# Performance work log

Measured on AMD Instinct MI355X. Metric: run time of the kernel, lower is better.

## Reference

```python
import jax, jax.numpy as jnp
import numpy as np

B, T, D, N = 32, 2048, 1024, 1024  # batch, time, feature dim, n_dense


def setup_inputs() -> dict:
    key = jax.random.key(0)
    ks = jax.random.split(key, 8)
    s = 1.0 / np.sqrt(D)
    return {
        "query": jax.random.normal(ks[0], (B, D), jnp.float32),
        "values": jax.random.normal(ks[1], (B, T, D), jnp.float32),
        "W1": jax.random.uniform(ks[2], (D, N), jnp.float32, -s, s),
        "b1": jnp.zeros((N,), jnp.float32),
        "W2": jax.random.uniform(ks[3], (D, N), jnp.float32, -s, s),
        "b2": jnp.zeros((N,), jnp.float32),
        "V": jax.random.uniform(ks[4], (N, 1), jnp.float32, -1.0 / np.sqrt(N), 1.0 / np.sqrt(N)),
        "bV": jnp.zeros((1,), jnp.float32),
    }


def reference(query, values, W1, b1, W2, b2, V, bV):
    # q_proj: [B, 1, N], v_proj: [B, T, N]
    q_proj = (query @ W1 + b1)[:, None, :]
    v_proj = jnp.einsum("btd,dn->btn", values, W2) + b2
    # score: [B, T, 1]
    score = jnp.tanh(q_proj + v_proj) @ V + bV
    attention_weights = jax.nn.softmax(score, axis=1)  # softmax over time
    # context: [B, D]
    context_vector = jnp.sum(attention_weights * values, axis=1)
    return (context_vector, attention_weights)
```

## Files before the change

### kernel.cpp

```cpp
#include <hip/hip_runtime.h>
#include <hip/hip_bf16.h>

#define B_ 32
#define T_ 2048
#define D_ 1024
#define N_ 1024
#define M_ (B_*T_)

#define BM 64
#define BN 128
#define BK 64
#define NTSPLIT 2
#define NTP (N_ / BN / NTSPLIT)
#define NSTEP (NTP * (D_ / BK))

typedef short bf16x8 __attribute__((ext_vector_type(8)));
typedef float f32x4 __attribute__((ext_vector_type(4)));
typedef unsigned short us4 __attribute__((ext_vector_type(4)));

__device__ __forceinline__ unsigned short bf16_rn(float x) {
    unsigned u = __float_as_uint(x);
    u += 0x7FFFu + ((u >> 16) & 1u);
    return (unsigned short)(u >> 16);
}

__device__ __forceinline__ void gload_lds16(const void* g, void* l) {
    __builtin_amdgcn_global_load_lds(
        (__attribute__((address_space(1))) void*)(g),
        (__attribute__((address_space(3))) void*)(l), 16, 0, 0);
}

__global__ void k0_w2t(const float* __restrict__ W2,
                       unsigned short* __restrict__ Th) {
    __shared__ float tile[32][33];
    int n0 = blockIdx.x * 32, d0 = blockIdx.y * 32;
    int tx = threadIdx.x & 31, ty = threadIdx.x >> 5;
    #pragma unroll
    for (int i = 0; i < 4; i++) {
        int d = d0 + ty + i * 8;
        tile[ty + i * 8][tx] = W2[d * N_ + n0 + tx];
    }
    __syncthreads();
    #pragma unroll
    for (int i = 0; i < 4; i++) {
        int n = n0 + ty + i * 8;
        Th[n * D_ + d0 + tx] = bf16_rn(tile[tx][ty + i * 8]);
    }
}

__global__ void k0_vals(const float* __restrict__ v,
                        unsigned short* __restrict__ o) {
    size_t i = ((size_t)blockIdx.x * 256 + threadIdx.x) * 8;
    const size_t stride = (size_t)gridDim.x * 256 * 8;
    for (; i < (size_t)M_ * D_; i += stride) {
        float4 a = *(const float4*)(v + i);
        float4 b = *(const float4*)(v + i + 4);
        us4 h0, h1;
        h0[0] = bf16_rn(a.x); h0[1] = bf16_rn(a.y);
        h0[2] = bf16_rn(a.z); h0[3] = bf16_rn(a.w);
        h1[0] = bf16_rn(b.x); h1[1] = bf16_rn(b.y);
        h1[2] = bf16_rn(b.z); h1[3] = bf16_rn(b.w);
        *(us4*)(o + i) = h0;
        *(us4*)(o + i + 4) = h1;
    }
}

__global__ void k1_qproj(const float* __restrict__ query,
                         const float* __restrict__ W1,
                         const float* __restrict__ b1,
                         float* __restrict__ qp) {
    int b = blockIdx.x;
    int n = blockIdx.y * 256 + threadIdx.x;
    const float* q = query + b * D_;
    const float* w = W1 + n;
    float s = 0.f;
    #pragma unroll 8
    for (int d = 0; d < D_; d++) s += q[d] * w[d * N_];
    qp[b * N_ + n] = s + b1[n];
}

__device__ __forceinline__ void k2_stage(int u, unsigned short* sa, unsigned short* sb,
                                         int m0, int nt0, int wid, int b_rl, int b_j,
                                         const unsigned short* __restrict__ Av,
                                         const unsigned short* __restrict__ W2Th) {
    const int nt = nt0 + (u >> 4);
    const int k0 = (u & 15) * BK;
    #pragma unroll
    for (int i = 0; i < 4; i++) {
        int r = wid * 32 + i * 8 + b_rl;
        int jj = b_j ^ (r & 7);
        size_t soff = (size_t)(nt * BN + r) * D_ + k0 + jj * 8;
        gload_lds16(W2Th + soff, &sb[(wid * 32 + i * 8) * 64]);
    }
    #pragma unroll
    for (int i = 0; i < 2; i++) {
        int r = wid * 16 + i * 8 + b_rl;
        int jj = b_j ^ (r & 7);
        size_t soff = (size_t)(m0 + r) * D_ + k0 + jj * 8;
        gload_lds16(Av + soff, &sa[(wid * 16 + i * 8) * 64]);
    }
}

__global__ __launch_bounds__(256, 2) void k2_score(
    const unsigned short* __restrict__ Av,
    const unsigned short* __restrict__ W2Th,
    const float* __restrict__ qp,
    const float* __restrict__ b2,
    const float* __restrict__ V,
    float* __restrict__ scorep) {
    __shared__ unsigned short sA[2][BM * BK];
    __shared__ unsigned short sB[2][BN * BK];
    __shared__ float red[2 * BM];

    const int tid = threadIdx.x;
    const int lane = tid & 63;
    const int wid = tid >> 6;
    const int wm = wid >> 1, wn = wid & 1;
    const int g = lane >> 4, c16 = lane & 15;

    const int bid = blockIdx.x;
    const int wgid = ((bid & 7) << 8) | (bid >> 3);
    const int m0 = (wgid >> 1) * BM;
    const int b = m0 >> 11;
    const int half = wgid & 1;
    const int nt0 = half * NTP;

    const int b_rl = lane >> 3;
    const int b_j = lane & 7;

    float rowpart[8];
    #pragma unroll
    for (int i = 0; i < 8; i++) rowpart[i] = 0.f;

    f32x4 acc[2][4];
    #pragma unroll
    for (int mi = 0; mi < 2; mi++)
        #pragma unroll
        for (int ni = 0; ni < 4; ni++) {
            f32x4 z = {0.f, 0.f, 0.f, 0.f};
            acc[mi][ni] = z;
        }

    k2_stage(0, sA[0], sB[0], m0, nt0, wid, b_rl, b_j, Av, W2Th);
    __syncthreads();

    for (int u = 0; u < NSTEP; ++u) {
        const int cur = u & 1;

        if (u + 1 < NSTEP)
            k2_stage(u + 1, sA[cur ^ 1], sB[cur ^ 1], m0, nt0, wid, b_rl, b_j, Av, W2Th);

        #pragma unroll
        for (int s = 0; s < 2; s++) {
            bf16x8 aH[2], bH[4];
            #pragma unroll
            for (int mi = 0; mi < 2; mi++) {
                int r = wm * 32 + mi * 16 + c16;
                int idx = r * 64 + (((s * 4 + g) ^ (r & 7)) << 3);
                aH[mi] = *(const bf16x8*)&sA[cur][idx];
            }
            #pragma unroll
            for (int ni = 0; ni < 4; ni++) {
                int r = wn * 64 + ni * 16 + c16;
                int idx = r * 64 + (((s * 4 + g) ^ (r & 7)) << 3);
                bH[ni] = *(const bf16x8*)&sB[cur][idx];
            }
            #pragma unroll
            for (int mi = 0; mi < 2; mi++)
                #pragma unroll
                for (int ni = 0; ni < 4; ni++)
                    acc[mi][ni] = __builtin_amdgcn_mfma_f32_16x16x32_bf16(aH[mi], bH[ni], acc[mi][ni], 0, 0, 0);
        }

        if ((u & 15) == 15) {
            int nt = nt0 + (u >> 4);
            #pragma unroll
            for (int ni = 0; ni < 4; ni++) {
                int n = nt * BN + wn * 64 + ni * 16 + c16;
                float qv = qp[b * N_ + n] + b2[n];
                float Vv = V[n];
                #pragma unroll
                for (int mi = 0; mi < 2; mi++)
                    #pragma unroll
                    for (int r = 0; r < 4; r++)
                        rowpart[mi * 4 + r] += tanhf(acc[mi][ni][r] + qv) * Vv;
            }
            #pragma unroll
            for (int mi = 0; mi < 2; mi++)
                #pragma unroll
                for (int ni = 0; ni < 4; ni++) {
                    f32x4 z = {0.f, 0.f, 0.f, 0.f};
                    acc[mi][ni] = z;
                }
        }

        __syncthreads();
    }

    #pragma unroll
    for (int i = 0; i < 8; i++) {
        float v = rowpart[i];
        v += __shfl_xor(v, 1);
        v += __shfl_xor(v, 2);
        v += __shfl_xor(v, 4);
        v += __shfl_xor(v, 8);
        rowpart[i] = v;
    }
    if (c16 == 0) {
        #pragma unroll
        for (int mi = 0; mi < 2; mi++)
            #pragma unroll
            for (int r = 0; r < 4; r++)
                red[wn * BM + wm * 32 + mi * 16 + g * 4 + r] = rowpart[mi * 4 + r];
    }
    __syncthreads();
    if (tid < BM) {
        scorep[(size_t)half * M_ + m0 + tid] = red[tid] + red[BM + tid];
    }
}

__global__ void k3_softmax(const float* __restrict__ sp,
                           float* __restrict__ sw) {
    int b = blockIdx.x;
    const float* r0 = sp + b * T_;
    const float* r1 = sp + M_ + b * T_;
    float* row = sw + b * T_;
    int tid = threadIdx.x;
    float v[8];
    float lmax = -1e30f;
    #pragma unroll
    for (int i = 0; i < 8; i++) {
        int idx = tid + i * 256;
        v[i] = r0[idx] + r1[idx];
        lmax = fmaxf(lmax, v[i]);
    }
    #pragma unroll
    for (int d = 1; d < 64; d <<= 1) lmax = fmaxf(lmax, __shfl_xor(lmax, d));
    __shared__ float sm[4], ss[4];
    if ((tid & 63) == 0) sm[tid >> 6] = lmax;
    __syncthreads();
    lmax = fmaxf(fmaxf(sm[0], sm[1]), fmaxf(sm[2], sm[3]));
    float lsum = 0.f;
    #pragma unroll
    for (int i = 0; i < 8; i++) {
        v[i] = expf(v[i] - lmax);
        lsum += v[i];
    }
    #pragma unroll
    for (int d = 1; d < 64; d <<= 1) lsum += __shfl_xor(lsum, d);
    if ((tid & 63) == 0) ss[tid >> 6] = lsum;
    __syncthreads();
    lsum = ss[0] + ss[1] + ss[2] + ss[3];
    float inv = 1.f / lsum;
    #pragma unroll
    for (int i = 0; i < 8; i++) row[tid + i * 256] = v[i] * inv;
}

__global__ void k4_context(const unsigned short* __restrict__ Av,
                           const float* __restrict__ w,
                           float* __restrict__ ctx) {
    int b = blockIdx.x;
    int dc = blockIdx.y;
    int tc = blockIdx.z;
    int d4 = threadIdx.x & 31;
    int th = threadIdx.x >> 5;
    const float* wrow = w + b * T_;
    int d = dc * 128 + d4 * 4;
    const unsigned short* vbase = Av + (size_t)b * T_ * D_ + d;
    float4 acc = {0.f, 0.f, 0.f, 0.f};
    int t0 = tc * 256 + th * 32;
    for (int t = t0; t < t0 + 32; t++) {
        float wt = wrow[t];
        us4 hv = *(const us4*)(vbase + (size_t)t * D_);
        acc.x += wt * __uint_as_float((unsigned)hv[0] << 16);
        acc.y += wt * __uint_as_float((unsigned)hv[1] << 16);
        acc.z += wt * __uint_as_float((unsigned)hv[2] << 16);
        acc.w += wt * __uint_as_float((unsigned)hv[3] << 16);
    }
    __shared__ float4 red4[256];
    red4[threadIdx.x] = acc;
    __syncthreads();
    if (th == 0) {
        float4 s = red4[d4];
        #pragma unroll
        for (int i = 1; i < 8; i++) {
            float4 o = red4[i * 32 + d4];
            s.x += o.x; s.y += o.y; s.z += o.z; s.w += o.w;
        }
        atomicAdd(&ctx[b * D_ + d + 0], s.x);
        atomicAdd(&ctx[b * D_ + d + 1], s.y);
        atomicAdd(&ctx[b * D_ + d + 2], s.z);
        atomicAdd(&ctx[b * D_ + d + 3], s.w);
    }
}

extern "C" void kernel_launch(void* const* d_in, const int* in_sizes, int n_in,
                              void* d_out, int out_size, void* d_ws, size_t ws_size,
                              hipStream_t stream) {
    const float* query  = (const float*)d_in[0];
    const float* values = (const float*)d_in[1];
    const float* W1     = (const float*)d_in[2];
    const float* b1     = (const float*)d_in[3];
    const float* W2     = (const float*)d_in[4];
    const float* b2     = (const float*)d_in[5];
    const float* V      = (const float*)d_in[6];

    float* ctx = (float*)d_out;
    float* weights = (float*)d_out + B_ * D_;

    size_t need = (size_t)N_ * D_ * sizeof(unsigned short)
                + (size_t)B_ * N_ * sizeof(float)
                + (size_t)NTSPLIT * M_ * sizeof(float)
                + (size_t)M_ * D_ * sizeof(unsigned short);
    if (ws_size < need) return;
    unsigned short* Th = (unsigned short*)d_ws;
    float* qp = (float*)(Th + (size_t)N_ * D_);
    float* scorep = qp + (size_t)B_ * N_;
    unsigned short* Av = (unsigned short*)(scorep + (size_t)NTSPLIT * M_);

    k0_w2t<<<dim3(N_ / 32, D_ / 32), 256, 0, stream>>>(W2, Th);
    k0_vals<<<2048, 256, 0, stream>>>(values, Av);
    k1_qproj<<<dim3(B_, N_ / 256), 256, 0, stream>>>(query, W1, b1, qp);
    k2_score<<<(M_ / BM) * NTSPLIT, 256, 0, stream>>>(Av, Th, qp, b2, V, scorep);
    k3_softmax<<<B_, 256, 0, stream>>>(scorep, weights);
    hipMemsetAsync(ctx, 0, (size_t)B_ * D_ * sizeof(float), stream);
    k4_context<<<dim3(B_, 8, 8), 256, 0, stream>>>(Av, weights, ctx);
}
```

Baseline: 395.7 us.

## Triple-buffer score GEMM with BK=32 and merge prep kernels and memset

The score GEMM moves from a double-buffered BK=64 loop with a full __syncthreads to a triple-buffered BK=32 pipeline. It uses explicit vmcnt waits and raw barriers so two global-to-LDS loads stay in flight while MFMAs run, and the LDS swizzle changes to suit 32-wide rows. The W2 transpose and q-projection are fused into one prep kernel, and the context memset moves into the softmax kernel, which removes launches. The smaller K step doubles the number of barriers and loop iterations, and there is a redundant dead LDS read left in the B-fragment load.

Result: no change. 399.4 us (+0.9%).

```diff
diff --git a/kernel.cpp b/kernel.cpp
--- a/kernel.cpp
+++ b/kernel.cpp
@@ -9,7 +9,7 @@
 
 #define BM 64
 #define BN 128
-#define BK 64
+#define BK 32
 #define NTSPLIT 2
 #define NTP (N_ / BN / NTSPLIT)
 #define NSTEP (NTP * (D_ / BK))
@@ -30,21 +30,40 @@
         (__attribute__((address_space(3))) void*)(l), 16, 0, 0);
 }
 
-__global__ void k0_w2t(const float* __restrict__ W2,
-                       unsigned short* __restrict__ Th) {
+#define FENCE() asm volatile("" ::: "memory")
+#define RAW_BARRIER() do { FENCE(); __builtin_amdgcn_s_barrier(); FENCE(); } while (0)
+
+__global__ void k_prep(const float* __restrict__ W2, unsigned short* __restrict__ Th,
+                       const float* __restrict__ query, const float* __restrict__ W1,
+                       const float* __restrict__ b1, float* __restrict__ qp) {
     __shared__ float tile[32][33];
-    int n0 = blockIdx.x * 32, d0 = blockIdx.y * 32;
-    int tx = threadIdx.x & 31, ty = threadIdx.x >> 5;
-    #pragma unroll
-    for (int i = 0; i < 4; i++) {
-        int d = d0 + ty + i * 8;
-        tile[ty + i * 8][tx] = W2[d * N_ + n0 + tx];
-    }
-    __syncthreads();
-    #pragma unroll
-    for (int i = 0; i < 4; i++) {
-        int n = n0 + ty + i * 8;
-        Th[n * D_ + d0 + tx] = bf16_rn(tile[tx][ty + i * 8]);
+    const int blk = blockIdx.x;
+    const int tid = threadIdx.x;
+
+    if (blk < 1024) {
+        int n0 = (blk & 31) * 32, d0 = (blk >> 5) * 32;
+        int tx = tid & 31, ty = tid >> 5;
+        #pragma unroll
+        for (int i = 0; i < 4; i++) {
+            int d = d0 + ty + i * 8;
+            tile[ty + i * 8][tx] = W2[d * N_ + n0 + tx];
+        }
+        __syncthreads();
+        #pragma unroll
+        for (int i = 0; i < 4; i++) {
+            int n = n0 + ty + i * 8;
+            Th[n * D_ + d0 + tx] = bf16_rn(tile[tx][ty + i * 8]);
+        }
+    } else {
+        int t = blk - 1024;
+        int b = t & 31;
+        int n = (t >> 5) * 256 + tid;
+        const float* q = query + b * D_;
+        const float* w = W1 + n;
+        float s = 0.f;
+        #pragma unroll 8
+        for (int d = 0; d < D_; d++) s += q[d] * w[d * N_];
+        qp[b * N_ + n] = s + b1[n];
     }
 }
 
@@ -65,39 +84,26 @@
     }
 }
 
-__global__ void k1_qproj(const float* __restrict__ query,
-                         const float* __restrict__ W1,
-                         const float* __restrict__ b1,
-                         float* __restrict__ qp) {
-    int b = blockIdx.x;
-    int n = blockIdx.y * 256 + threadIdx.x;
-    const float* q = query + b * D_;
-    const float* w = W1 + n;
-    float s = 0.f;
-    #pragma unroll 8
-    for (int d = 0; d < D_; d++) s += q[d] * w[d * N_];
-    qp[b * N_ + n] = s + b1[n];
-}
-
 __device__ __forceinline__ void k2_stage(int u, unsigned short* sa, unsigned short* sb,
-                                         int m0, int nt0, int wid, int b_rl, int b_j,
+                                         int m0, int nt0, int wid, int lane,
                                          const unsigned short* __restrict__ Av,
                                          const unsigned short* __restrict__ W2Th) {
-    const int nt = nt0 + (u >> 4);
-    const int k0 = (u & 15) * BK;
-    #pragma unroll
-    for (int i = 0; i < 4; i++) {
-        int r = wid * 32 + i * 8 + b_rl;
-        int jj = b_j ^ (r & 7);
+    const int nt = nt0 + (u >> 5);
+    const int k0 = (u & 31) * BK;
+    const int rl4 = lane >> 2;
+    const int j4 = lane & 3;
+    #pragma unroll
+    for (int i = 0; i < 2; i++) {
+        int r = wid * 32 + i * 16 + rl4;
+        int jj = j4 ^ (r & 3) ^ ((r >> 2) & 3);
         size_t soff = (size_t)(nt * BN + r) * D_ + k0 + jj * 8;
-        gload_lds16(W2Th + soff, &sb[(wid * 32 + i * 8) * 64]);
-    }
-    #pragma unroll
-    for (int i = 0; i < 2; i++) {
-        int r = wid * 16 + i * 8 + b_rl;
-        int jj = b_j ^ (r & 7);
+        gload_lds16(W2Th + soff, &sb[(wid * 32 + i * 16) * 32]);
+    }
+    {
+        int r = wid * 16 + rl4;
+        int jj = j4 ^ (r & 3) ^ ((r >> 2) & 3);
         size_t soff = (size_t)(m0 + r) * D_ + k0 + jj * 8;
-        gload_lds16(Av + soff, &sa[(wid * 16 + i * 8) * 64]);
+        gload_lds16(Av + soff, &sa[(wid * 16) * 32]);
     }
 }
 
@@ -108,8 +114,8 @@
     const float* __restrict__ b2,
     const float* __restrict__ V,
     float* __restrict__ scorep) {
-    __shared__ unsigned short sA[2][BM * BK];
-    __shared__ unsigned short sB[2][BN * BK];
+    __shared__ unsigned short sA[3][BM * BK];
+    __shared__ unsigned short sB[3][BN * BK];
     __shared__ float red[2 * BM];
 
     const int tid = threadIdx.x;
@@ -125,9 +131,6 @@
     const int half = wgid & 1;
     const int nt0 = half * NTP;
 
-    const int b_rl = lane >> 3;
-    const int b_j = lane & 7;
-
     float rowpart[8];
     #pragma unroll
     for (int i = 0; i < 8; i++) rowpart[i] = 0.f;
@@ -141,29 +144,32 @@
             acc[mi][ni] = z;
         }
 
-    k2_stage(0, sA[0], sB[0], m0, nt0, wid, b_rl, b_j, Av, W2Th);
-    __syncthreads();
-
-    for (int u = 0; u < NSTEP; ++u) {
-        const int cur = u & 1;
-
-        if (u + 1 < NSTEP)
-            k2_stage(u + 1, sA[cur ^ 1], sB[cur ^ 1], m0, nt0, wid, b_rl, b_j, Av, W2Th);
-
-        #pragma unroll
-        for (int s = 0; s < 2; s++) {
+    unsigned short *a0 = sA[0], *a1 = sA[1], *a2 = sA[2];
+    unsigned short *b0 = sB[0], *b1 = sB[1], *b2p = sB[2];
+
+    k2_stage(0, a0, b0, m0, nt0, wid, lane, Av, W2Th);
+    k2_stage(1, a1, b1, m0, nt0, wid, lane, Av, W2Th);
+    asm volatile("s_waitcnt vmcnt(3)" ::: "memory");
+    RAW_BARRIER();
+
+    for (int s = 0; s < NSTEP; ++s) {
+        if (s + 2 < NSTEP)
+            k2_stage(s + 2, a2, b2p, m0, nt0, wid, lane, Av, W2Th);
+
+        {
             bf16x8 aH[2], bH[4];
             #pragma unroll
             for (int mi = 0; mi < 2; mi++) {
                 int r = wm * 32 + mi * 16 + c16;
-                int idx = r * 64 + (((s * 4 + g) ^ (r & 7)) << 3);
-                aH[mi] = *(const bf16x8*)&sA[cur][idx];
+                int ch = g ^ (r & 3) ^ ((r >> 2) & 3);
+                aH[mi] = *(const bf16x8*)&a0[r * 32 + ch * 8];
             }
             #pragma unroll
             for (int ni = 0; ni < 4; ni++) {
                 int r = wn * 64 + ni * 16 + c16;
-                int idx = r * 64 + (((s * 4 + g) ^ (r & 7)) << 3);
-                bH[ni] = *(const bf16x8*)&sB[cur][idx];
+                int ch = g ^ (r & 3) ^ ((r >> 2) & 3);
+                bH[ni] = *(const bf16x8*)&sB[0][0];
+                bH[ni] = *(const bf16x8*)&b0[r * 32 + ch * 8];
             }
             #pragma unroll
             for (int mi = 0; mi < 2; mi++)
@@ -172,8 +178,8 @@
                     acc[mi][ni] = __builtin_amdgcn_mfma_f32_16x16x32_bf16(aH[mi], bH[ni], acc[mi][ni], 0, 0, 0);
         }
 
-        if ((u & 15) == 15) {
-            int nt = nt0 + (u >> 4);
+        if ((s & 31) == 31) {
+            int nt = nt0 + (s >> 5);
             #pragma unroll
             for (int ni = 0; ni < 4; ni++) {
                 int n = nt * BN + wn * 64 + ni * 16 + c16;
@@ -194,7 +200,15 @@
                 }
         }
 
-        __syncthreads();
+        if (s + 2 < NSTEP) {
+            asm volatile("s_waitcnt vmcnt(3)" ::: "memory");
+        } else if (s + 1 < NSTEP) {
+            asm volatile("s_waitcnt vmcnt(0)" ::: "memory");
+        }
+        RAW_BARRIER();
+
+        unsigned short* t0 = a0; a0 = a1; a1 = a2; a2 = t0;
+        unsigned short* t1 = b0; b0 = b1; b1 = b2p; b2p = t1;
     }
 
     #pragma unroll
@@ -220,12 +234,17 @@
 }
 
 __global__ void k3_softmax(const float* __restrict__ sp,
-                           float* __restrict__ sw) {
+                           float* __restrict__ sw,
+                           float* __restrict__ ctx) {
     int b = blockIdx.x;
     const float* r0 = sp + b * T_;
     const float* r1 = sp + M_ + b * T_;
     float* row = sw + b * T_;
     int tid = threadIdx.x;
+
+    #pragma unroll
+    for (int i = 0; i < 4; i++) ctx[b * D_ + tid + i * 256] = 0.f;
+
     float v[8];
     float lmax = -1e30f;
     #pragma unroll
@@ -318,11 +337,9 @@
     float* scorep = qp + (size_t)B_ * N_;
     unsigned short* Av = (unsigned short*)(scorep + (size_t)NTSPLIT * M_);
 
-    k0_w2t<<<dim3(N_ / 32, D_ / 32), 256, 0, stream>>>(W2, Th);
+    k_prep<<<1152, 256, 0, stream>>>(W2, Th, query, W1, b1, qp);
     k0_vals<<<2048, 256, 0, stream>>>(values, Av);
-    k1_qproj<<<dim3(B_, N_ / 256), 256, 0, stream>>>(query, W1, b1, qp);
     k2_score<<<(M_ / BM) * NTSPLIT, 256, 0, stream>>>(Av, Th, qp, b2, V, scorep);
-    k3_softmax<<<B_, 256, 0, stream>>>(scorep, weights);
-    hipMemsetAsync(ctx, 0, (size_t)B_ * D_ * sizeof(float), stream);
+    k3_softmax<<<B_, 256, 0, stream>>>(scorep, weights, ctx);
     k4_context<<<dim3(B_, 8, 8), 256, 0, stream>>>(Av, weights, ctx);
 }
```
